# Kernel tuning notes

Measured on AMD Instinct MI355X. Metric: run time of the kernel, lower is better.

## Reference

```python
import jax, jax.numpy as jnp
import numpy as np


def setup_inputs() -> dict:
    N, E, D, C = 100000, 100000, 512, 512
    key = jax.random.key(0)
    k = jax.random.split(key, 6)
    x = jax.random.normal(k[0], (N, D), dtype=jnp.float32)
    W = jax.random.normal(k[1], (D, 3 * C), dtype=jnp.float32) * (1.0 / np.sqrt(D))
    bias = jax.random.normal(k[2], (C,), dtype=jnp.float32) * (1.0 / np.sqrt(C))
    eta = jax.random.uniform(k[3], (E, 3, 1), dtype=jnp.float32)
    src = jax.random.randint(k[4], (E,), 0, N, dtype=jnp.int32)
    dst = jax.random.randint(k[5], (E,), 0, N, dtype=jnp.int32)
    return {"x": x, "W": W, "bias": bias, "eta": eta, "src": src, "dst": dst}


def reference(x, W, bias, eta, src, dst):
    N = x.shape[0]
    C = bias.shape[0]
    # projection: [N, D] @ [D, 3C] -> [N, 3, C]
    h = jnp.matmul(x, W).reshape(N, 3, C)
    # message: src node state scaled by per-edge eta [E,3,1]
    msg = h[src] * eta  # [E, 3, C]
    # reduce: sum messages into destination nodes (nodes w/o in-edges -> 0)
    agg = jax.ops.segment_sum(msg, dst, num_segments=N)  # [N, 3, C]
    # sum over the 3 positional slots, add bias, tanh
    return jnp.tanh(agg.sum(axis=1) + bias)
```

## Files before the change

kernel.cpp:

```cpp
#include <hip/hip_runtime.h>

typedef _Float16 half_t;
typedef __attribute__((ext_vector_type(8))) _Float16 half8;
typedef __attribute__((ext_vector_type(4))) float floatx4;

#define BM 256
#define BN 256
#define BK 64

__global__ void cvt_w_kernel(const float* __restrict__ W, half_t* __restrict__ Wt,
                             const float* __restrict__ bias, float* __restrict__ tb,
                             int D, int C, int total) {
    int idx = blockIdx.x * blockDim.x + threadIdx.x;
    if (idx >= total) return;
    if (idx < C) {
        float ex = __expf(2.0f * bias[idx]);
        tb[idx] = 1.0f - 2.0f / (ex + 1.0f);
    }
    int c = idx / 1536;
    int r = idx - c * 1536;
    int s = r >> 9;
    int d = r & 511;
    Wt[idx] = (half_t)W[(long)d * 1536 + s * 512 + c];
}

__global__ void hist_kernel(const int* __restrict__ dst, int* __restrict__ deg, int E) {
    int e = blockIdx.x * blockDim.x + threadIdx.x;
    if (e < E) atomicAdd(&deg[dst[e]], 1);
}

__global__ void scan_partial2_kernel(const int* __restrict__ deg,
                                     int* __restrict__ bsum, int* __restrict__ bsum2, int n) {
    __shared__ int wsum[4], wsum2[4];
    int t = threadIdx.x, lane = t & 63, w = t >> 6;
    int base = blockIdx.x * 1024 + t * 4;
    int s = 0, s2 = 0;
#pragma unroll
    for (int j = 0; j < 4; ++j) {
        int i = base + j;
        if (i < n) { int d = deg[i]; s += d; s2 += (d > 0); }
    }
#pragma unroll
    for (int o = 1; o < 64; o <<= 1) { s += __shfl_xor(s, o); s2 += __shfl_xor(s2, o); }
    if (lane == 0) { wsum[w] = s; wsum2[w] = s2; }
    __syncthreads();
    if (t == 0) {
        bsum[blockIdx.x]  = wsum[0]  + wsum[1]  + wsum[2]  + wsum[3];
        bsum2[blockIdx.x] = wsum2[0] + wsum2[1] + wsum2[2] + wsum2[3];
    }
}

__device__ int exscan_wave128(int* arr, int nb, int lane) {
    int a0 = (lane < nb) ? arr[lane] : 0;
    int a1 = (64 + lane < nb) ? arr[64 + lane] : 0;
    int s0 = a0, s1 = a1;
#pragma unroll
    for (int o = 1; o < 64; o <<= 1) {
        int t0 = __shfl_up(s0, o); if (lane >= o) s0 += t0;
        int t1 = __shfl_up(s1, o); if (lane >= o) s1 += t1;
    }
    s1 += __shfl(s0, 63);
    int tot = __shfl(s1, 63);
    if (lane < nb) arr[lane] = s0 - a0;
    if (64 + lane < nb) arr[64 + lane] = s1 - a1;
    return tot;
}

__global__ void scan_bsums2_kernel(int* __restrict__ bsum, int* __restrict__ bsum2,
                                   int nb, int* __restrict__ mc) {
    int lane = threadIdx.x & 63;
    if (nb <= 128) {
        exscan_wave128(bsum, nb, lane);
        int tot = exscan_wave128(bsum2, nb, lane);
        if (lane == 0) *mc = tot;
    } else if (lane == 0) {
        int acc = 0, acc2 = 0;
        for (int i = 0; i < nb; ++i) {
            int v = bsum[i];  bsum[i] = acc;   acc += v;
            int v2 = bsum2[i]; bsum2[i] = acc2; acc2 += v2;
        }
        *mc = acc2;
    }
}

__global__ void scan_final2_kernel(const int* __restrict__ deg,
                                   const int* __restrict__ bsum, const int* __restrict__ bsum2,
                                   int* __restrict__ off, int* __restrict__ rank,
                                   int* __restrict__ nodeid, int n) {
    __shared__ int wsum[4], wsum2[4];
    int t = threadIdx.x, lane = t & 63, w = t >> 6;
    int base = blockIdx.x * 1024 + t * 4;
    int v[4]; int s = 0, s2 = 0;
#pragma unroll
    for (int j = 0; j < 4; ++j) {
        int i = base + j;
        v[j] = (i < n) ? deg[i] : 0;
        s += v[j]; s2 += (v[j] > 0);
    }
    int sc = s, sc2 = s2;
#pragma unroll
    for (int o = 1; o < 64; o <<= 1) {
        int u  = __shfl_up(sc, o);  if (lane >= o) sc  += u;
        int u2 = __shfl_up(sc2, o); if (lane >= o) sc2 += u2;
    }
    if (lane == 63) { wsum[w] = sc; wsum2[w] = sc2; }
    __syncthreads();
    int woff = 0, woff2 = 0;
    for (int i = 0; i < w; ++i) { woff += wsum[i]; woff2 += wsum2[i]; }
    int ex  = bsum[blockIdx.x]  + woff  + (sc  - s);
    int ex2 = bsum2[blockIdx.x] + woff2 + (sc2 - s2);
#pragma unroll
    for (int j = 0; j < 4; ++j) {
        int i = base + j;
        if (i < n) {
            off[i] = ex;
            if (v[j] > 0) { rank[i] = ex2; nodeid[ex2] = i; ex2++; }
            ex += v[j];
        }
    }
}

__global__ void scatter_kernel(const int* __restrict__ dst, const int* __restrict__ src,
                               const float* __restrict__ eta,
                               const int* __restrict__ off, int* __restrict__ cursor,
                               int* __restrict__ srcs, floatx4* __restrict__ etas, int E) {
    int e = blockIdx.x * blockDim.x + threadIdx.x;
    if (e >= E) return;
    int d = dst[e];
    int p = off[d] + atomicAdd(&cursor[d], 1);
    srcs[p] = src[e];
    floatx4 et;
    et[0] = eta[3 * e + 0]; et[1] = eta[3 * e + 1]; et[2] = eta[3 * e + 2]; et[3] = 0.0f;
    etas[p] = et;
}

__global__ __launch_bounds__(256) void aggx_kernel(
    const float* __restrict__ x, const int* __restrict__ srcs,
    const floatx4* __restrict__ etas, const int* __restrict__ off,
    const int* __restrict__ deg, const int* __restrict__ rank,
    const float* __restrict__ tb, float* __restrict__ out,
    half_t* __restrict__ Z, int N, int D, int C)
{
    int node = blockIdx.x * 4 + (threadIdx.x >> 6);
    if (node >= N) return;
    int lane = threadIdx.x & 63;
    int d = deg[node];
    if (d == 0) {
        float* o = out + (long)node * C;
        for (int c0 = lane * 8; c0 < C; c0 += 64 * 8) {
            floatx4 v0 = *(const floatx4*)(tb + c0);
            floatx4 v1 = *(const floatx4*)(tb + c0 + 4);
            __builtin_nontemporal_store(v0, (floatx4*)(o + c0));
            __builtin_nontemporal_store(v1, (floatx4*)(o + c0 + 4));
        }
        return;
    }

    float a0[8] = {}, a1[8] = {}, a2[8] = {};
    int start = off[node];
    for (int q = 0; q < d; ++q) {
        int s = srcs[start + q];
        floatx4 et = etas[start + q];
        const float* xr = x + (long)s * D + lane * 8;
        floatx4 v0 = *(const floatx4*)xr;
        floatx4 v1 = *(const floatx4*)(xr + 4);
#pragma unroll
        for (int j = 0; j < 4; ++j) {
            a0[j] += et[0] * v0[j]; a0[j + 4] += et[0] * v1[j];
            a1[j] += et[1] * v0[j]; a1[j + 4] += et[1] * v1[j];
            a2[j] += et[2] * v0[j]; a2[j + 4] += et[2] * v1[j];
        }
    }
    half_t* zr = Z + (long)rank[node] * (3 * D) + lane * 8;
    half8 h0, h1, h2;
#pragma unroll
    for (int j = 0; j < 8; ++j) { h0[j] = (half_t)a0[j]; h1[j] = (half_t)a1[j]; h2[j] = (half_t)a2[j]; }
    *(half8*)zr = h0;
    *(half8*)(zr + D) = h1;
    *(half8*)(zr + 2 * D) = h2;
}

__global__ __launch_bounds__(512, 2) void gemm_tanh_kernel(
    const half_t* __restrict__ A,
    const half_t* __restrict__ Bt,
    const float* __restrict__ bias,
    const int* __restrict__ mc_ptr,
    const int* __restrict__ nodeid,
    float* __restrict__ out,
    int K, int C)
{
    __shared__ half_t As[2][2][128 * 64];
    __shared__ half_t Bs[2][2][128 * 64];

    const int Mc = *mc_ptr;
    const int ncol = C / BN;
    const int T = ((Mc + BM - 1) / BM) * ncol;
    const int b = blockIdx.x;
    if (b >= T) return;
    const int qq = T >> 3, rem = T & 7;
    const int xcd = b & 7, ib = b >> 3;
    const int wg = (xcd < rem ? xcd * (qq + 1) : rem * (qq + 1) + (xcd - rem) * qq) + ib;
    const int n0 = (wg % ncol) * BN;
    const int m0 = (wg / ncol) * BM;

    const int t    = threadIdx.x;
    const int lane = t & 63;
    const int wave = t >> 6;
    const int wm   = (wave >> 2) * 128;
    const int wn   = (wave & 3) * 64;
    const int hA   = wave >> 2;
    const int hB   = (wave & 3) >> 1;
    const int cb   = (wave & 1) * 64;

    const int r1 = t >> 3;
    const int k8 = (((t & 7) ^ ((t >> 3) & 7))) * 8;
    const long gA0 = (long)(m0 + r1)       * K + k8;
    const long gA1 = (long)(m0 + 64 + r1)  * K + k8;
    const long gA2 = (long)(m0 + 128 + r1) * K + k8;
    const long gA3 = (long)(m0 + 192 + r1) * K + k8;
    const long gB0 = (long)(n0 + r1)       * K + k8;
    const long gB1 = (long)(n0 + 64 + r1)  * K + k8;
    const long gB2 = (long)(n0 + 128 + r1) * K + k8;
    const long gB3 = (long)(n0 + 192 + r1) * K + k8;

    floatx4 acc[8][4] = {};

    const int aBase = (lane & 15) * 64;
    const int bBase = (cb + (lane & 15)) * 64;
    const int c0 = (((lane >> 4)) ^ (lane & 7)) * 8;
    const int c1 = (((lane >> 4) + 4) ^ (lane & 7)) * 8;

#define STAGE(buf, ktk)                                                                     \
    do {                                                                                    \
        __builtin_amdgcn_global_load_lds(                                                   \
            (const __attribute__((address_space(1))) void*)(A + gA0 + (ktk)),               \
            (__attribute__((address_space(3))) void*)(&As[buf][0][t * 8]), 16, 0, 0);       \
        __builtin_amdgcn_global_load_lds(                                                   \
            (const __attribute__((address_space(1))) void*)(A + gA1 + (ktk)),               \
            (__attribute__((address_space(3))) void*)(&As[buf][0][(512 + t) * 8]), 16, 0, 0); \
        __builtin_amdgcn_global_load_lds(                                                   \
            (const __attribute__((address_space(1))) void*)(A + gA2 + (ktk)),               \
            (__attribute__((address_space(3))) void*)(&As[buf][1][t * 8]), 16, 0, 0);       \
        __builtin_amdgcn_global_load_lds(                                                   \
            (const __attribute__((address_space(1))) void*)(A + gA3 + (ktk)),               \
            (__attribute__((address_space(3))) void*)(&As[buf][1][(512 + t) * 8]), 16, 0, 0); \
        __builtin_amdgcn_global_load_lds(                                                   \
            (const __attribute__((address_space(1))) void*)(Bt + gB0 + (ktk)),              \
            (__attribute__((address_space(3))) void*)(&Bs[buf][0][t * 8]), 16, 0, 0);       \
        __builtin_amdgcn_global_load_lds(                                                   \
            (const __attribute__((address_space(1))) void*)(Bt + gB1 + (ktk)),              \
            (__attribute__((address_space(3))) void*)(&Bs[buf][0][(512 + t) * 8]), 16, 0, 0); \
        __builtin_amdgcn_global_load_lds(                                                   \
            (const __attribute__((address_space(1))) void*)(Bt + gB2 + (ktk)),              \
            (__attribute__((address_space(3))) void*)(&Bs[buf][1][t * 8]), 16, 0, 0);       \
        __builtin_amdgcn_global_load_lds(                                                   \
            (const __attribute__((address_space(1))) void*)(Bt + gB3 + (ktk)),              \
            (__attribute__((address_space(3))) void*)(&Bs[buf][1][(512 + t) * 8]), 16, 0, 0); \
    } while (0)

#define COMPUTE(buf)                                                                        \
    do {                                                                                    \
        const half_t* Ab = &As[buf][hA][0];                                                 \
        const half_t* Bb = &Bs[buf][hB][0];                                                 \
        half8 a[8], bf[4];                                                                  \
        _Pragma("unroll") for (int i = 0; i < 8; ++i)                                       \
            a[i] = *(const half8*)&Ab[aBase + i * 1024 + c0];                               \
        _Pragma("unroll") for (int j = 0; j < 4; ++j)                                       \
            bf[j] = *(const half8*)&Bb[bBase + j * 1024 + c0];                              \
        _Pragma("unroll") for (int i = 0; i < 8; ++i)                                       \
            _Pragma("unroll") for (int j = 0; j < 4; ++j)                                   \
                acc[i][j] = __builtin_amdgcn_mfma_f32_16x16x32_f16(a[i], bf[j],             \
                                                                   acc[i][j], 0, 0, 0);    \
        _Pragma("unroll") for (int i = 0; i < 8; ++i)                                       \
            a[i] = *(const half8*)&Ab[aBase + i * 1024 + c1];                               \
        _Pragma("unroll") for (int j = 0; j < 4; ++j)                                       \
            bf[j] = *(const half8*)&Bb[bBase + j * 1024 + c1];                              \
        _Pragma("unroll") for (int i = 0; i < 8; ++i)                                       \
            _Pragma("unroll") for (int j = 0; j < 4; ++j)                                   \
                acc[i][j] = __builtin_amdgcn_mfma_f32_16x16x32_f16(a[i], bf[j],             \
                                                                   acc[i][j], 0, 0, 0);    \
    } while (0)

    const int nt = K / BK;
    STAGE(0, 0);
    for (int kt = 0; kt < nt; ++kt) {
        if (kt + 1 < nt) {
            STAGE((kt + 1) & 1, (kt + 1) * BK);
            asm volatile("s_waitcnt vmcnt(8)" ::: "memory");
        } else {
            asm volatile("s_waitcnt vmcnt(0)" ::: "memory");
        }
        __builtin_amdgcn_sched_barrier(0);
        __builtin_amdgcn_s_barrier();
        __builtin_amdgcn_sched_barrier(0);
        COMPUTE(kt & 1);
        __builtin_amdgcn_sched_barrier(0);
        __builtin_amdgcn_s_barrier();
        __builtin_amdgcn_sched_barrier(0);
    }

#undef STAGE
#undef COMPUTE

    const int col0 = lane & 15;
    const int rbase = (lane >> 4) * 4;
    float bj[4];
#pragma unroll
    for (int j = 0; j < 4; ++j)
        bj[j] = bias[n0 + wn + col0 + j * 16];
#pragma unroll
    for (int i = 0; i < 8; ++i) {
#pragma unroll
        for (int rr = 0; rr < 4; ++rr) {
            int crow = m0 + wm + i * 16 + rbase + rr;
            if (crow >= Mc) continue;
            long base = (long)nodeid[crow] * C + n0 + wn + col0;
#pragma unroll
            for (int j = 0; j < 4; ++j) {
                float xv = acc[i][j][rr] + bj[j];
                float ex = __expf(2.0f * xv);
                __builtin_nontemporal_store(1.0f - 2.0f / (ex + 1.0f), &out[base + j * 16]);
            }
        }
    }
}

extern "C" void kernel_launch(void* const* d_in, const int* in_sizes, int n_in,
                              void* d_out, int out_size, void* d_ws, size_t ws_size,
                              hipStream_t stream) {
    const float* x    = (const float*)d_in[0];
    const float* W    = (const float*)d_in[1];
    const float* bias = (const float*)d_in[2];
    const float* eta  = (const float*)d_in[3];
    const int*   src  = (const int*)d_in[4];
    const int*   dst  = (const int*)d_in[5];
    float* out = (float*)d_out;

    const int  C   = in_sizes[2];
    const int  C3  = 3 * C;
    const int  D   = in_sizes[1] / C3;
    const long xcount = in_sizes[0];
    const int  N   = (int)(xcount / D);
    const int  E   = in_sizes[4];
    const int  K   = 3 * D;
    const int  Npad = ((N + BM - 1) / BM) * BM;
    const int  nb  = (N + 1023) / 1024;
    const size_t nbPad = (size_t)((nb + 3) & ~3);

    auto alignup = [](size_t v) { return (v + 15) & ~(size_t)15; };

    char* ws = (char*)d_ws;
    size_t o = 0;
    half_t* Z    = (half_t*)(ws + o); o += (size_t)Npad * K * sizeof(half_t);
    half_t* Wt_h = (half_t*)(ws + o); o += (size_t)C * K * sizeof(half_t);
    int* deg     = (int*)(ws + o);    o += (size_t)N * sizeof(int);
    int* cursor  = (int*)(ws + o);    o += (size_t)N * sizeof(int);
    int* off     = (int*)(ws + o);    o += (size_t)N * sizeof(int);
    int* rank    = (int*)(ws + o);    o += (size_t)N * sizeof(int);
    int* nodeid  = (int*)(ws + o);    o += (size_t)N * sizeof(int);
    int* srcs    = (int*)(ws + o);    o += (size_t)E * sizeof(int);
    o = alignup(o);
    floatx4* etas = (floatx4*)(ws + o); o += (size_t)E * sizeof(floatx4);
    int* bsum    = (int*)(ws + o);    o += nbPad * sizeof(int);
    int* bsum2   = (int*)(ws + o);    o += nbPad * sizeof(int);
    int* mc      = (int*)(ws + o);    o += 4 * sizeof(int);
    float* tb    = (float*)(ws + o);  o += (size_t)C * sizeof(float);

    hipMemsetAsync(deg, 0, 2 * (size_t)N * sizeof(int), stream);
    cvt_w_kernel<<<(C * K + 255) / 256, 256, 0, stream>>>(W, Wt_h, bias, tb, D, C, C * K);
    hist_kernel<<<(E + 255) / 256, 256, 0, stream>>>(dst, deg, E);
    scan_partial2_kernel<<<nb, 256, 0, stream>>>(deg, bsum, bsum2, N);
    scan_bsums2_kernel<<<1, 64, 0, stream>>>(bsum, bsum2, nb, mc);
    scan_final2_kernel<<<nb, 256, 0, stream>>>(deg, bsum, bsum2, off, rank, nodeid, N);
    scatter_kernel<<<(E + 255) / 256, 256, 0, stream>>>(dst, src, eta, off, cursor, srcs, etas, E);
    aggx_kernel<<<(N + 3) / 4, 256, 0, stream>>>(x, srcs, etas, off, deg, rank, tb, out, Z, N, D, C);
    {
        const int nwg = (Npad / BM) * (C / BN);
        gemm_tanh_kernel<<<nwg, 512, 0, stream>>>(Z, Wt_h, bias, mc, nodeid, out, K, C);
    }
}
```

Before: 543.4 us.

## Split GEMM main loop into four quadrant phases interleaving global loads with MFMA

The GEMM k-loop is restructured. Instead of staging a whole tile and then computing all 8x4 MFMAs, each iteration runs four quadrant phases. Each phase reads part of the A/B fragments from LDS, issues a quarter of the next tile's global-to-LDS loads, and runs its MFMAs at raised wave priority (s_setprio). The aim is to hide global and LDS latency behind matrix work and cut the live fragment registers. The cost is many more workgroup barriers per k-step and extra LDS fragment re-reads.

```diff
diff --git a/kernel.cpp b/kernel.cpp
--- a/kernel.cpp
+++ b/kernel.cpp
@@ -225,82 +225,105 @@
 
     floatx4 acc[8][4] = {};
 
-    const int aBase = (lane & 15) * 64;
-    const int bBase = (cb + (lane & 15)) * 64;
-    const int c0 = (((lane >> 4)) ^ (lane & 7)) * 8;
-    const int c1 = (((lane >> 4) + 4) ^ (lane & 7)) * 8;
-
-#define STAGE(buf, ktk)                                                                     \
+    const int aRow = lane & 15;
+    const int bRow = cb + (lane & 15);
+    const int c0e = (((lane >> 4)) ^ (lane & 7)) * 8;
+    const int c1e = (((lane >> 4) + 4) ^ (lane & 7)) * 8;
+
+    half8 aK0[4], aK1[4];
+    half8 bK0[2], bK1[2];
+
+#define GLL(gp, lp)                                                          \
+    __builtin_amdgcn_global_load_lds(                                        \
+        (const __attribute__((address_space(1))) void*)(gp),                 \
+        (__attribute__((address_space(3))) void*)(lp), 16, 0, 0)
+
+#define STAGE_A0(buf, ktk) do { GLL(A + gA0 + (ktk), &As[buf][0][t * 8]);     \
+                                GLL(A + gA1 + (ktk), &As[buf][0][(512 + t) * 8]); } while (0)
+#define STAGE_A1(buf, ktk) do { GLL(A + gA2 + (ktk), &As[buf][1][t * 8]);     \
+                                GLL(A + gA3 + (ktk), &As[buf][1][(512 + t) * 8]); } while (0)
+#define STAGE_B0(buf, ktk) do { GLL(Bt + gB0 + (ktk), &Bs[buf][0][t * 8]);    \
+                                GLL(Bt + gB1 + (ktk), &Bs[buf][0][(512 + t) * 8]); } while (0)
+#define STAGE_B1(buf, ktk) do { GLL(Bt + gB2 + (ktk), &Bs[buf][1][t * 8]);    \
+                                GLL(Bt + gB3 + (ktk), &Bs[buf][1][(512 + t) * 8]); } while (0)
+
+#define READ_A(p, ih)                                                                       \
     do {                                                                                    \
-        __builtin_amdgcn_global_load_lds(                                                   \
-            (const __attribute__((address_space(1))) void*)(A + gA0 + (ktk)),               \
-            (__attribute__((address_space(3))) void*)(&As[buf][0][t * 8]), 16, 0, 0);       \
-        __builtin_amdgcn_global_load_lds(                                                   \
-            (const __attribute__((address_space(1))) void*)(A + gA1 + (ktk)),               \
-            (__attribute__((address_space(3))) void*)(&As[buf][0][(512 + t) * 8]), 16, 0, 0); \
-        __builtin_amdgcn_global_load_lds(                                                   \
-            (const __attribute__((address_space(1))) void*)(A + gA2 + (ktk)),               \
-            (__attribute__((address_space(3))) void*)(&As[buf][1][t * 8]), 16, 0, 0);       \
-        __builtin_amdgcn_global_load_lds(                                                   \
-            (const __attribute__((address_space(1))) void*)(A + gA3 + (ktk)),               \
-            (__attribute__((address_space(3))) void*)(&As[buf][1][(512 + t) * 8]), 16, 0, 0); \
-        __builtin_amdgcn_global_load_lds(                                                   \
-            (const __attribute__((address_space(1))) void*)(Bt + gB0 + (ktk)),              \
-            (__attribute__((address_space(3))) void*)(&Bs[buf][0][t * 8]), 16, 0, 0);       \
-        __builtin_amdgcn_global_load_lds(                                                   \
-            (const __attribute__((address_space(1))) void*)(Bt + gB1 + (ktk)),              \
-            (__attribute__((address_space(3))) void*)(&Bs[buf][0][(512 + t) * 8]), 16, 0, 0); \
-        __builtin_amdgcn_global_load_lds(                                                   \
-            (const __attribute__((address_space(1))) void*)(Bt + gB2 + (ktk)),              \
-            (__attribute__((address_space(3))) void*)(&Bs[buf][1][t * 8]), 16, 0, 0);       \
-        __builtin_amdgcn_global_load_lds(                                                   \
-            (const __attribute__((address_space(1))) void*)(Bt + gB3 + (ktk)),              \
-            (__attribute__((address_space(3))) void*)(&Bs[buf][1][(512 + t) * 8]), 16, 0, 0); \
+        const half_t* Ab_ = &As[p][hA][0];                                                  \
+        _Pragma("unroll") for (int i2 = 0; i2 < 4; ++i2) {                                  \
+            aK0[i2] = *(const half8*)&Ab_[(aRow + (4 * (ih) + i2) * 16) * 64 + c0e];        \
+            aK1[i2] = *(const half8*)&Ab_[(aRow + (4 * (ih) + i2) * 16) * 64 + c1e];        \
+        }                                                                                   \
     } while (0)
 
-#define COMPUTE(buf)                                                                        \
+#define READ_B(p, jh)                                                                       \
     do {                                                                                    \
-        const half_t* Ab = &As[buf][hA][0];                                                 \
-        const half_t* Bb = &Bs[buf][hB][0];                                                 \
-        half8 a[8], bf[4];                                                                  \
-        _Pragma("unroll") for (int i = 0; i < 8; ++i)                                       \
-            a[i] = *(const half8*)&Ab[aBase + i * 1024 + c0];                               \
-        _Pragma("unroll") for (int j = 0; j < 4; ++j)                                       \
-            bf[j] = *(const half8*)&Bb[bBase + j * 1024 + c0];                              \
-        _Pragma("unroll") for (int i = 0; i < 8; ++i)                                       \
-            _Pragma("unroll") for (int j = 0; j < 4; ++j)                                   \
-                acc[i][j] = __builtin_amdgcn_mfma_f32_16x16x32_f16(a[i], bf[j],             \
-                                                                   acc[i][j], 0, 0, 0);    \
-        _Pragma("unroll") for (int i = 0; i < 8; ++i)                                       \
-            a[i] = *(const half8*)&Ab[aBase + i * 1024 + c1];                               \
-        _Pragma("unroll") for (int j = 0; j < 4; ++j)                                       \
-            bf[j] = *(const half8*)&Bb[bBase + j * 1024 + c1];                              \
-        _Pragma("unroll") for (int i = 0; i < 8; ++i)                                       \
-            _Pragma("unroll") for (int j = 0; j < 4; ++j)                                   \
-                acc[i][j] = __builtin_amdgcn_mfma_f32_16x16x32_f16(a[i], bf[j],             \
-                                                                   acc[i][j], 0, 0, 0);    \
+        const half_t* Bb_ = &Bs[p][hB][0];                                                  \
+        _Pragma("unroll") for (int j2 = 0; j2 < 2; ++j2) {                                  \
+            bK0[j2] = *(const half8*)&Bb_[(bRow + (2 * (jh) + j2) * 16) * 64 + c0e];        \
+            bK1[j2] = *(const half8*)&Bb_[(bRow + (2 * (jh) + j2) * 16) * 64 + c1e];        \
+        }                                                                                   \
     } while (0)
 
+#define MFMA_Q(ih, jh)                                                                      \
+    do {                                                                                    \
+        _Pragma("unroll") for (int i2 = 0; i2 < 4; ++i2)                                    \
+            _Pragma("unroll") for (int j2 = 0; j2 < 2; ++j2) {                              \
+                acc[4 * (ih) + i2][2 * (jh) + j2] = __builtin_amdgcn_mfma_f32_16x16x32_f16( \
+                    aK0[i2], bK0[j2], acc[4 * (ih) + i2][2 * (jh) + j2], 0, 0, 0);          \
+                acc[4 * (ih) + i2][2 * (jh) + j2] = __builtin_amdgcn_mfma_f32_16x16x32_f16( \
+                    aK1[i2], bK1[j2], acc[4 * (ih) + i2][2 * (jh) + j2], 0, 0, 0);          \
+            }                                                                               \
+    } while (0)
+
+#define SCHED __builtin_amdgcn_sched_barrier(0)
+#define BAR   __builtin_amdgcn_s_barrier()
+#define LGKM0 asm volatile("s_waitcnt lgkmcnt(0)" ::: "memory")
+
     const int nt = K / BK;
-    STAGE(0, 0);
+    STAGE_A0(0, 0); STAGE_A1(0, 0); STAGE_B0(0, 0); STAGE_B1(0, 0);
+
     for (int kt = 0; kt < nt; ++kt) {
-        if (kt + 1 < nt) {
-            STAGE((kt + 1) & 1, (kt + 1) * BK);
-            asm volatile("s_waitcnt vmcnt(8)" ::: "memory");
-        } else {
-            asm volatile("s_waitcnt vmcnt(0)" ::: "memory");
-        }
-        __builtin_amdgcn_sched_barrier(0);
-        __builtin_amdgcn_s_barrier();
-        __builtin_amdgcn_sched_barrier(0);
-        COMPUTE(kt & 1);
-        __builtin_amdgcn_sched_barrier(0);
-        __builtin_amdgcn_s_barrier();
-        __builtin_amdgcn_sched_barrier(0);
-    }
-
-#undef STAGE
-#undef COMPUTE
+        const int p  = kt & 1;
+        const int pn = p ^ 1;
+        const int kn = (kt + 1) * BK;
+        const bool more = (kt + 1 < nt);
+
+        if (more) { STAGE_A0(pn, kn); asm volatile("s_waitcnt vmcnt(2)" ::: "memory"); }
+        else      { asm volatile("s_waitcnt vmcnt(0)" ::: "memory"); }
+        SCHED; BAR; SCHED;
+        READ_A(p, 0); READ_B(p, 0);
+        LGKM0; SCHED;
+        __builtin_amdgcn_s_setprio(1); MFMA_Q(0, 0); __builtin_amdgcn_s_setprio(0); SCHED;
+        BAR;
+        READ_B(p, 1);
+        if (more) STAGE_A1(pn, kn);
+        SCHED; BAR; LGKM0; SCHED;
+        __builtin_amdgcn_s_setprio(1); MFMA_Q(0, 1); __builtin_amdgcn_s_setprio(0); SCHED;
+        BAR;
+        READ_A(p, 1);
+        if (more) STAGE_B0(pn, kn);
+        SCHED; BAR; LGKM0; SCHED;
+        __builtin_amdgcn_s_setprio(1); MFMA_Q(1, 1); __builtin_amdgcn_s_setprio(0); SCHED;
+        BAR;
+        READ_B(p, 0);
+        if (more) STAGE_B1(pn, kn);
+        SCHED; BAR; LGKM0; SCHED;
+        __builtin_amdgcn_s_setprio(1); MFMA_Q(1, 0); __builtin_amdgcn_s_setprio(0); SCHED;
+        BAR;
+    }
+
+#undef GLL
+#undef STAGE_A0
+#undef STAGE_A1
+#undef STAGE_B0
+#undef STAGE_B1
+#undef READ_A
+#undef READ_B
+#undef MFMA_Q
+#undef SCHED
+#undef BAR
+#undef LGKM0
 
     const int col0 = lane & 15;
     const int rbase = (lane >> 4) * 4;
```

Result: slower. 556.1 us (+2.3%).
